# Kernel optimization log

Measured on AMD Instinct MI355X. Metric: run time of the kernel, lower is better.

Reference implementation:

```python
import jax, jax.numpy as jnp
import numpy as np
from math import pi

TWO_PI = 2.0 * pi

def ringify(x):
    return (x + pi) % TWO_PI - pi

def complex_mean(x, axes):
    dir_x = ringify(jnp.cos(x)).sum(axis=axes)
    dir_y = jnp.sin(x).sum(axis=axes)
    return jnp.arctan2(dir_y, dir_x)

def extract_patches(x, k, s):
    # x: (B, C, H, W) -> (B, Ho, Wo, C, k, k)
    B, C, H, W = x.shape
    Ho = (H - k) // s + 1
    Wo = (W - k) // s + 1
    idx_h = jnp.arange(Ho)[:, None] * s + jnp.arange(k)[None, :]  # (Ho, k)
    idx_w = jnp.arange(Wo)[:, None] * s + jnp.arange(k)[None, :]  # (Wo, k)
    # advanced indexing on dims 2,3 with broadcast shape (Ho, Wo, k, k)
    p = x[:, :, idx_h[:, None, :, None], idx_w[None, :, None, :]]  # (B, C, Ho, Wo, k, k)
    return p.transpose(0, 2, 3, 1, 4, 5)

def ring_conv2d(x, weight, kernel_size, stride):
    # x: (B, C, H, W); weight: (O, C, k, k) -> out: (B, Ho, Wo, O)
    patches = extract_patches(x, kernel_size, stride)            # (B,Ho,Wo,C,k,k)
    w = weight.transpose(1, 2, 3, 0)                              # (C,k,k,O)
    diff = ringify(patches[..., None] - w)                        # (B,Ho,Wo,C,k,k,O)
    return complex_mean(diff, axes=(-4, -3, -2))                  # (B,Ho,Wo,O)

def setup_inputs() -> dict:
    key = jax.random.key(0)
    k1, k2, k3, k4 = jax.random.split(key, 4)
    return {
        "x": jax.random.normal(k1, (4096, 1, 28, 28), dtype=jnp.float32),
        "conv1_weight": jax.random.normal(k2, (4, 1, 2, 2), dtype=jnp.float32),
        "conv2_weight": jax.random.normal(k3, (8, 4, 4, 4), dtype=jnp.float32),
        "ff_weight": jax.random.normal(k4, (288, 10), dtype=jnp.float32),
    }

def reference(x, conv1_weight, conv2_weight, ff_weight):
    h = ringify(x).reshape(-1, 1, 28, 28)
    h = ring_conv2d(h, conv1_weight, kernel_size=2, stride=2)     # (B,14,14,4)
    h = h.transpose(0, 3, 1, 2)                                   # (B,4,14,14)
    h = ring_conv2d(h, conv2_weight, kernel_size=4, stride=2)     # (B,6,6,8)
    h = h.reshape(h.shape[0], -1)                                 # (B,288)
    h = complex_mean(ringify(h[:, :, None] - ff_weight), axes=(-2,))  # (B,10)
    return jnp.sin(h)
```

## Files before the change

kernel.cpp:

```cpp
#include <hip/hip_runtime.h>

#define WT_W1 0
#define WT_FF 528
#define WT_B2_BYTES (3408 * 8)

typedef _Float16 h2  __attribute__((ext_vector_type(2)));
typedef _Float16 v8h __attribute__((ext_vector_type(8)));
typedef float    f4  __attribute__((ext_vector_type(4)));

__device__ __forceinline__ float fdot2(unsigned a, unsigned b, float c) {
    return __builtin_amdgcn_fdot2(__builtin_bit_cast(h2, a),
                                  __builtin_bit_cast(h2, b), c, false);
}
__device__ __forceinline__ unsigned packh2(float x, float y) {
    h2 h; h.x = (_Float16)x; h.y = (_Float16)y;
    return __builtin_bit_cast(unsigned, h);
}

__global__ void ringnn_setup(const float* __restrict__ w1,
                             const float* __restrict__ w2,
                             const float* __restrict__ ffw,
                             uint2* __restrict__ wt) {
    int t = blockIdx.x * blockDim.x + threadIdx.x;
    if (t < 3408) {
        float a;
        if (t < 16)        a = w1[t];
        else if (t < 528)  a = w2[t - 16];
        else               a = ffw[t - 528];
        float s, c;
        __sincosf(a, &s, &c);
        uint2 v;
        v.x = packh2(c, s);
        v.y = packh2(-s, c);
        wt[t] = v;
    } else if (t < 3408 + 256) {
        const int e  = t - 3408;
        const int nn = e & 15;
        const int dy = (e >> 4) & 3;
        const int c  = e >> 6;
        const int o  = nn >> 1;
        unsigned d[4];
        #pragma unroll
        for (int dx = 0; dx < 4; ++dx) {
            float a = w2[o * 64 + c * 16 + dy * 4 + dx];
            float s, cc;
            __sincosf(a, &s, &cc);
            d[dx] = (nn & 1) ? packh2(-s, cc) : packh2(cc, s);
        }
        uint4* Bt = (uint4*)((char*)wt + WT_B2_BYTES);
        Bt[e] = make_uint4(d[0], d[1], d[2], d[3]);
    }
}

__global__ __launch_bounds__(256) void ringnn_main(
    const float* __restrict__ x,
    const uint2* __restrict__ wt,
    float* __restrict__ out)
{
    __shared__ __align__(16) unsigned cs1[2][784];
    __shared__ __align__(16) unsigned cs2[2][288];

    const int t     = threadIdx.x;
    const int wave  = t >> 6;
    const int lane  = t & 63;
    const int img   = t >> 7;
    const int tid   = t & 127;
    const int b0    = blockIdx.x * 2;
    const float* xb = x + (b0 + img) * 784;

    for (int pos = tid; pos < 196; pos += 128) {
        const int i = pos / 14;
        const int j = pos - i * 14;
        const float* px = xb + (2 * i) * 28 + 2 * j;
        float2 p0 = *(const float2*)(px);
        float2 p1 = *(const float2*)(px + 28);
        float s0, c0, s1, c1, s2, c2, s3, c3;
        __sincosf(p0.x, &s0, &c0);
        __sincosf(p0.y, &s1, &c1);
        __sincosf(p1.x, &s2, &c2);
        __sincosf(p1.y, &s3, &c3);
        unsigned v0 = packh2(c0, s0), v1 = packh2(c1, s1);
        unsigned v2 = packh2(c2, s2), v3 = packh2(c3, s3);
        #pragma unroll
        for (int o = 0; o < 4; ++o) {
            uint2 wa = wt[WT_W1 + o * 4 + 0], wb = wt[WT_W1 + o * 4 + 1];
            uint2 wc = wt[WT_W1 + o * 4 + 2], wd = wt[WT_W1 + o * 4 + 3];
            float X = 0.f, Y = 0.f;
            X = fdot2(v0, wa.x, X); Y = fdot2(v0, wa.y, Y);
            X = fdot2(v1, wb.x, X); Y = fdot2(v1, wb.y, Y);
            X = fdot2(v2, wc.x, X); Y = fdot2(v2, wc.y, Y);
            X = fdot2(v3, wd.x, X); Y = fdot2(v3, wd.y, Y);
            float rinv = rsqrtf(fmaxf(fmaf(X, X, Y * Y), 1e-30f));
            cs1[img][o * 196 + pos] = packh2(X * rinv, Y * rinv);
        }
    }

    const int n    = lane & 15;
    const int quad = lane >> 4;
    const uint4* Bt = (const uint4*)((const char*)wt + WT_B2_BYTES);
    uint4 bf0 = Bt[lane];
    uint4 bf1 = Bt[64 + lane];
    uint4 bf2 = Bt[128 + lane];
    uint4 bf3 = Bt[192 + lane];

    __syncthreads();

    const unsigned* c1 = &cs1[0][0];
    for (int tile = wave; tile < 5; tile += 4) {
        const int p  = tile * 16 + n;
        const int pc = (p < 72) ? p : 71;
        const int im = (pc >= 36) ? 1 : 0;
        const int ps = pc - im * 36;
        const int i  = ps / 6;
        const int j  = ps - i * 6;
        const unsigned base = (unsigned)(im * 784 + (2 * i + quad) * 14 + 2 * j);
        f4 acc = {0.f, 0.f, 0.f, 0.f};
        #pragma unroll
        for (int c = 0; c < 4; ++c) {
            uint2 lo = *(const uint2*)(c1 + base + c * 196);
            uint2 hi = *(const uint2*)(c1 + base + c * 196 + 2);
            uint4 a4 = make_uint4(lo.x, lo.y, hi.x, hi.y);
            v8h av = __builtin_bit_cast(v8h, a4);
            v8h bv = __builtin_bit_cast(v8h, (c == 0) ? bf0 : (c == 1) ? bf1
                                              : (c == 2) ? bf2 : bf3);
            acc = __builtin_amdgcn_mfma_f32_16x16x32_f16(av, bv, acc, 0, 0, 0);
        }
        float pr0 = __shfl_xor(acc[0], 1);
        float pr1 = __shfl_xor(acc[1], 1);
        float pr2 = __shfl_xor(acc[2], 1);
        float pr3 = __shfl_xor(acc[3], 1);
        if (!(n & 1)) {
            const int o = n >> 1;
            float Xs[4] = {acc[0], acc[1], acc[2], acc[3]};
            float Ys[4] = {pr0, pr1, pr2, pr3};
            #pragma unroll
            for (int r = 0; r < 4; ++r) {
                const int p2 = tile * 16 + quad * 4 + r;
                if (p2 < 72) {
                    const int im2 = (p2 >= 36) ? 1 : 0;
                    const int ps2 = p2 - im2 * 36;
                    float X = Xs[r], Y = Ys[r];
                    float rinv = rsqrtf(fmaxf(fmaf(X, X, Y * Y), 1e-30f));
                    cs2[im2][ps2 * 8 + o] = packh2(X * rinv, Y * rinv);
                }
            }
        }
    }
    __syncthreads();

    {
        const int half = wave & 1;
        const int nl   = lane / 12;
        const int g    = lane - nl * 12;
        float X = 0.f, Y = 0.f;
        if (nl < 5) {
            const int n3 = half * 5 + nl;
            #pragma unroll 6
            for (int k = 0; k < 24; ++k) {
                const int f = g + 12 * k;
                unsigned v = cs2[img][f];
                uint2 wvv = wt[WT_FF + f * 10 + n3];
                X = fdot2(v, wvv.x, X);
                Y = fdot2(v, wvv.y, Y);
            }
        }
        float qX = X + __shfl_down(X, 4) + __shfl_down(X, 8);
        float qY = Y + __shfl_down(Y, 4) + __shfl_down(Y, 8);
        float sX = qX + __shfl_down(qX, 1) + __shfl_down(qX, 2) + __shfl_down(qX, 3);
        float sY = qY + __shfl_down(qY, 1) + __shfl_down(qY, 2) + __shfl_down(qY, 3);
        if (g == 0 && nl < 5) {
            const int n3 = half * 5 + nl;
            float rinv = rsqrtf(fmaxf(fmaf(sX, sX, sY * sY), 1e-30f));
            out[(b0 + img) * 10 + n3] = sY * rinv;
        }
    }
}

extern "C" void kernel_launch(void* const* d_in, const int* in_sizes, int n_in,
                              void* d_out, int out_size, void* d_ws, size_t ws_size,
                              hipStream_t stream) {
    const float* x   = (const float*)d_in[0];
    const float* w1  = (const float*)d_in[1];
    const float* w2  = (const float*)d_in[2];
    const float* ffw = (const float*)d_in[3];
    uint2* wt = (uint2*)d_ws;
    float* o  = (float*)d_out;

    ringnn_setup<<<15, 256, 0, stream>>>(w1, w2, ffw, wt);
    ringnn_main<<<2048, 256, 0, stream>>>(x, wt, o);
}
```

Measured before the change: 76.32 us.

## Fuse weight-table setup into main kernel with per-block LDS tables

Drops the separate setup kernel. Each block now computes the sin/cos weight tables for conv1, conv2 (the MFMA B fragments) and the FF layer into shared memory. The FF table stores only (cos,sin), and the rotated (-sin,cos) copy is rebuilt with an alignbit and sign-flip. The conv1 input loads are issued before the table setup so their latency overlaps it, and work is spread across all 256 threads. This removes one kernel launch and the global weight-table traffic, but every block now redoes 2880+ sincos evaluations and uses about 17 KB more LDS, which may lower occupancy.

New measurement: 78.17 us. 1.02x slower.

```diff
diff --git a/kernel.cpp b/kernel.cpp
--- a/kernel.cpp
+++ b/kernel.cpp
@@ -1,8 +1,5 @@
 #include <hip/hip_runtime.h>
 
-#define WT_W1 0
-#define WT_FF 528
-#define WT_B2_BYTES (3408 * 8)
 
 typedef _Float16 h2  __attribute__((ext_vector_type(2)));
 typedef _Float16 v8h __attribute__((ext_vector_type(8)));
@@ -16,93 +13,119 @@
     h2 h; h.x = (_Float16)x; h.y = (_Float16)y;
     return __builtin_bit_cast(unsigned, h);
 }
-
-__global__ void ringnn_setup(const float* __restrict__ w1,
-                             const float* __restrict__ w2,
-                             const float* __restrict__ ffw,
-                             uint2* __restrict__ wt) {
-    int t = blockIdx.x * blockDim.x + threadIdx.x;
-    if (t < 3408) {
-        float a;
-        if (t < 16)        a = w1[t];
-        else if (t < 528)  a = w2[t - 16];
-        else               a = ffw[t - 528];
-        float s, c;
-        __sincosf(a, &s, &c);
-        uint2 v;
-        v.x = packh2(c, s);
-        v.y = packh2(-s, c);
-        wt[t] = v;
-    } else if (t < 3408 + 256) {
-        const int e  = t - 3408;
-        const int nn = e & 15;
-        const int dy = (e >> 4) & 3;
-        const int c  = e >> 6;
-        const int o  = nn >> 1;
-        unsigned d[4];
-        #pragma unroll
-        for (int dx = 0; dx < 4; ++dx) {
-            float a = w2[o * 64 + c * 16 + dy * 4 + dx];
-            float s, cc;
-            __sincosf(a, &s, &cc);
-            d[dx] = (nn & 1) ? packh2(-s, cc) : packh2(cc, s);
-        }
-        uint4* Bt = (uint4*)((char*)wt + WT_B2_BYTES);
-        Bt[e] = make_uint4(d[0], d[1], d[2], d[3]);
-    }
-}
-
-__global__ __launch_bounds__(256) void ringnn_main(
+__device__ __forceinline__ unsigned yrot(unsigned u) {
+    return __builtin_amdgcn_alignbit(u, u, 16) ^ 0x8000u;
+}
+
+__global__ __launch_bounds__(256) void ringnn_fused(
     const float* __restrict__ x,
-    const uint2* __restrict__ wt,
+    const float* __restrict__ w1,
+    const float* __restrict__ w2,
+    const float* __restrict__ ffw,
     float* __restrict__ out)
 {
     __shared__ __align__(16) unsigned cs1[2][784];
     __shared__ __align__(16) unsigned cs2[2][288];
-
-    const int t     = threadIdx.x;
-    const int wave  = t >> 6;
-    const int lane  = t & 63;
-    const int img   = t >> 7;
-    const int tid   = t & 127;
-    const int b0    = blockIdx.x * 2;
-    const float* xb = x + (b0 + img) * 784;
-
-    for (int pos = tid; pos < 196; pos += 128) {
-        const int i = pos / 14;
-        const int j = pos - i * 14;
-        const float* px = xb + (2 * i) * 28 + 2 * j;
-        float2 p0 = *(const float2*)(px);
-        float2 p1 = *(const float2*)(px + 28);
-        float s0, c0, s1, c1, s2, c2, s3, c3;
-        __sincosf(p0.x, &s0, &c0);
-        __sincosf(p0.y, &s1, &c1);
-        __sincosf(p1.x, &s2, &c2);
-        __sincosf(p1.y, &s3, &c3);
-        unsigned v0 = packh2(c0, s0), v1 = packh2(c1, s1);
-        unsigned v2 = packh2(c2, s2), v3 = packh2(c3, s3);
-        #pragma unroll
-        for (int o = 0; o < 4; ++o) {
-            uint2 wa = wt[WT_W1 + o * 4 + 0], wb = wt[WT_W1 + o * 4 + 1];
-            uint2 wc = wt[WT_W1 + o * 4 + 2], wd = wt[WT_W1 + o * 4 + 3];
-            float X = 0.f, Y = 0.f;
-            X = fdot2(v0, wa.x, X); Y = fdot2(v0, wa.y, Y);
-            X = fdot2(v1, wb.x, X); Y = fdot2(v1, wb.y, Y);
-            X = fdot2(v2, wc.x, X); Y = fdot2(v2, wc.y, Y);
-            X = fdot2(v3, wd.x, X); Y = fdot2(v3, wd.y, Y);
-            float rinv = rsqrtf(fmaxf(fmaf(X, X, Y * Y), 1e-30f));
-            cs1[img][o * 196 + pos] = packh2(X * rinv, Y * rinv);
-        }
-    }
+    __shared__ __align__(16) uint4    b2t[256];
+    __shared__ __align__(16) unsigned fft[2880];
+    __shared__ uint2 w1t[16];
+
+    const int t    = threadIdx.x;
+    const int wave = t >> 6;
+    const int lane = t & 63;
+    const int img  = t >> 7;
+    const int b0   = blockIdx.x * 2;
+
+    const int imA = (t >= 196) ? 1 : 0;
+    const int pA  = t - imA * 196;
+    const int iA  = pA / 14, jA = pA - iA * 14;
+    const float* pxA = x + (b0 + imA) * 784 + (2 * iA) * 28 + 2 * jA;
+    const float2 rA0 = *(const float2*)(pxA);
+    const float2 rA1 = *(const float2*)(pxA + 28);
+
+    const bool hasB = (t < 136);
+    const int pB  = t + 60;
+    const int iB  = pB / 14, jB = pB - iB * 14;
+    const float* pxB = x + (b0 + 1) * 784 + (2 * iB) * 28 + 2 * jB;
+    float2 rB0 = {0.f, 0.f}, rB1 = {0.f, 0.f};
+    if (hasB) { rB0 = *(const float2*)(pxB); rB1 = *(const float2*)(pxB + 28); }
+
+    if (t < 16) {
+        float s, c;
+        __sincosf(w1[t], &s, &c);
+        w1t[t] = make_uint2(packh2(c, s), packh2(-s, c));
+    }
+    {
+        const int nn = t & 15;
+        const int dy = (t >> 4) & 3;
+        const int cc = t >> 6;
+        const int o  = nn >> 1;
+        unsigned d[4];
+        #pragma unroll
+        for (int dx = 0; dx < 4; ++dx) {
+            float a = w2[o * 64 + cc * 16 + dy * 4 + dx];
+            float ss, cw;
+            __sincosf(a, &ss, &cw);
+            d[dx] = (nn & 1) ? packh2(-ss, cw) : packh2(cw, ss);
+        }
+        b2t[t] = make_uint4(d[0], d[1], d[2], d[3]);
+    }
+    for (int e = t; e < 2880; e += 256) {
+        float ss, cw;
+        __sincosf(ffw[e], &ss, &cw);
+        fft[e] = packh2(cw, ss);
+    }
+    __syncthreads();
 
     const int n    = lane & 15;
     const int quad = lane >> 4;
-    const uint4* Bt = (const uint4*)((const char*)wt + WT_B2_BYTES);
-    uint4 bf0 = Bt[lane];
-    uint4 bf1 = Bt[64 + lane];
-    uint4 bf2 = Bt[128 + lane];
-    uint4 bf3 = Bt[192 + lane];
-
+    uint4 bf0 = b2t[lane];
+    uint4 bf1 = b2t[64 + lane];
+    uint4 bf2 = b2t[128 + lane];
+    uint4 bf3 = b2t[192 + lane];
+
+    {
+        float s0, c0, s1, c1, s2, c2, s3, c3;
+        __sincosf(rA0.x, &s0, &c0);
+        __sincosf(rA0.y, &s1, &c1);
+        __sincosf(rA1.x, &s2, &c2);
+        __sincosf(rA1.y, &s3, &c3);
+        const unsigned u0 = packh2(c0, s0), u1 = packh2(c1, s1);
+        const unsigned u2 = packh2(c2, s2), u3 = packh2(c3, s3);
+        #pragma unroll
+        for (int o = 0; o < 4; ++o) {
+            const uint2 wa = w1t[o * 4 + 0], wb = w1t[o * 4 + 1];
+            const uint2 wc = w1t[o * 4 + 2], wd = w1t[o * 4 + 3];
+            float X = 0.f, Y = 0.f;
+            X = fdot2(u0, wa.x, X); Y = fdot2(u0, wa.y, Y);
+            X = fdot2(u1, wb.x, X); Y = fdot2(u1, wb.y, Y);
+            X = fdot2(u2, wc.x, X); Y = fdot2(u2, wc.y, Y);
+            X = fdot2(u3, wd.x, X); Y = fdot2(u3, wd.y, Y);
+            const float rinv = rsqrtf(fmaxf(fmaf(X, X, Y * Y), 1e-30f));
+            cs1[imA][o * 196 + pA] = packh2(X * rinv, Y * rinv);
+        }
+    }
+    if (hasB) {
+        float s0, c0, s1, c1, s2, c2, s3, c3;
+        __sincosf(rB0.x, &s0, &c0);
+        __sincosf(rB0.y, &s1, &c1);
+        __sincosf(rB1.x, &s2, &c2);
+        __sincosf(rB1.y, &s3, &c3);
+        const unsigned u0 = packh2(c0, s0), u1 = packh2(c1, s1);
+        const unsigned u2 = packh2(c2, s2), u3 = packh2(c3, s3);
+        #pragma unroll
+        for (int o = 0; o < 4; ++o) {
+            const uint2 wa = w1t[o * 4 + 0], wb = w1t[o * 4 + 1];
+            const uint2 wc = w1t[o * 4 + 2], wd = w1t[o * 4 + 3];
+            float X = 0.f, Y = 0.f;
+            X = fdot2(u0, wa.x, X); Y = fdot2(u0, wa.y, Y);
+            X = fdot2(u1, wb.x, X); Y = fdot2(u1, wb.y, Y);
+            X = fdot2(u2, wc.x, X); Y = fdot2(u2, wc.y, Y);
+            X = fdot2(u3, wd.x, X); Y = fdot2(u3, wd.y, Y);
+            const float rinv = rsqrtf(fmaxf(fmaf(X, X, Y * Y), 1e-30f));
+            cs1[1][o * 196 + pB] = packh2(X * rinv, Y * rinv);
+        }
+    }
     __syncthreads();
 
     const unsigned* c1 = &cs1[0][0];
@@ -152,18 +175,24 @@
         const int half = wave & 1;
         const int nl   = lane / 12;
         const int g    = lane - nl * 12;
-        float X = 0.f, Y = 0.f;
+        float XA = 0.f, YA = 0.f, XB = 0.f, YB = 0.f;
         if (nl < 5) {
             const int n3 = half * 5 + nl;
             #pragma unroll 6
-            for (int k = 0; k < 24; ++k) {
-                const int f = g + 12 * k;
-                unsigned v = cs2[img][f];
-                uint2 wvv = wt[WT_FF + f * 10 + n3];
-                X = fdot2(v, wvv.x, X);
-                Y = fdot2(v, wvv.y, Y);
+            for (int k = 0; k < 12; ++k) {
+                const int fA = g + 12 * k;
+                const int fB = fA + 144;
+                unsigned va = cs2[img][fA];
+                unsigned vb = cs2[img][fB];
+                unsigned ua = fft[fA * 10 + n3];
+                unsigned ub = fft[fB * 10 + n3];
+                XA = fdot2(va, ua, XA);
+                YA = fdot2(va, yrot(ua), YA);
+                XB = fdot2(vb, ub, XB);
+                YB = fdot2(vb, yrot(ub), YB);
             }
         }
+        float X = XA + XB, Y = YA + YB;
         float qX = X + __shfl_down(X, 4) + __shfl_down(X, 8);
         float qY = Y + __shfl_down(Y, 4) + __shfl_down(Y, 8);
         float sX = qX + __shfl_down(qX, 1) + __shfl_down(qX, 2) + __shfl_down(qX, 3);
@@ -183,9 +212,6 @@
     const float* w1  = (const float*)d_in[1];
     const float* w2  = (const float*)d_in[2];
     const float* ffw = (const float*)d_in[3];
-    uint2* wt = (uint2*)d_ws;
-    float* o  = (float*)d_out;
-
-    ringnn_setup<<<15, 256, 0, stream>>>(w1, w2, ffw, wt);
-    ringnn_main<<<2048, 256, 0, stream>>>(x, wt, o);
-}
+    (void)d_ws; (void)ws_size;
+    ringnn_fused<<<2048, 256, 0, stream>>>(x, w1, w2, ffw, (float*)d_out);
+}
```
